# Kernel optimization log

Hardware: AMD Instinct MI355X
Metric: run time of the kernel (lower is better)

Reference implementation:

```python
import jax, jax.numpy as jnp
import numpy as np

N_NODES = 100000
N_GRAPHS = 512
HID = 128
IN_DIM = 128
OUT_DIM = 10
N_EDGES = 1600000


def gcn_conv(x, src, dst, W, b, n):
    # PyG GCNConv: add self-loops, symmetric normalization D^-1/2 (A+I) D^-1/2, then linear.
    h = x @ W  # [N, H]
    deg = jnp.zeros((n,), h.dtype).at[dst].add(1.0) + 1.0  # +1 self-loop
    dinv = jax.lax.rsqrt(deg)
    norm = dinv[src] * dinv[dst]  # [E]
    agg = jnp.zeros_like(h).at[dst].add(h[src] * norm[:, None])
    agg = agg + h * (dinv * dinv)[:, None]  # self-loop messages
    return agg + b


def setup_inputs() -> dict:
    key = jax.random.key(0)
    ks = jax.random.split(key, 12)
    x = jax.random.normal(ks[0], (N_NODES, IN_DIM), jnp.float32)
    edge_index = jax.random.randint(ks[1], (2, N_EDGES), 0, N_NODES)
    batch = jnp.sort(jax.random.randint(ks[2], (N_NODES,), 0, N_GRAPHS))
    def lin(k, fan_in, shape):
        bound = 1.0 / np.sqrt(fan_in)
        return jax.random.uniform(k, shape, jnp.float32, -bound, bound)
    W1 = lin(ks[3], IN_DIM, (IN_DIM, HID)); b1 = lin(ks[4], IN_DIM, (HID,))
    W2 = lin(ks[5], HID, (HID, HID)); b2 = lin(ks[6], HID, (HID,))
    W3 = lin(ks[7], HID, (HID, HID)); b3 = lin(ks[8], HID, (HID,))
    Wc1 = lin(ks[9], 2 * HID, (2 * HID, HID)); bc1 = lin(ks[9], 2 * HID, (HID,))
    Wc2 = lin(ks[10], HID, (HID, OUT_DIM)); bc2 = lin(ks[11], HID, (OUT_DIM,))
    return {"x": x, "edge_index": edge_index, "batch": batch,
            "W1": W1, "b1": b1, "W2": W2, "b2": b2, "W3": W3, "b3": b3,
            "Wc1": Wc1, "bc1": bc1, "Wc2": Wc2, "bc2": bc2}


def reference(x, edge_index, batch, W1, b1, W2, b2, W3, b3, Wc1, bc1, Wc2, bc2):
    src, dst = edge_index[0], edge_index[1]
    n = x.shape[0]
    h = jax.nn.relu(gcn_conv(x, src, dst, W1, b1, n))
    h = jax.nn.relu(gcn_conv(h, src, dst, W2, b2, n))
    h = gcn_conv(h, src, dst, W3, b3, n)  # no relu after last conv
    # global mean pool
    sums = jax.ops.segment_sum(h, batch, num_segments=N_GRAPHS)
    cnt = jax.ops.segment_sum(jnp.ones((n,), h.dtype), batch, num_segments=N_GRAPHS)
    mean = sums / jnp.maximum(cnt, 1.0)[:, None]
    # global max pool
    mx = jax.ops.segment_max(h, batch, num_segments=N_GRAPHS)
    mx = jnp.where(jnp.isfinite(mx), mx, 0.0)
    g = jnp.concatenate([mean, mx], axis=1)  # [G, 2H]
    g = jax.nn.relu(g @ Wc1 + bc1)
    return g @ Wc2 + bc2
```

## Files before the change

kernel.cpp:

```cpp
#include <hip/hip_runtime.h>

#define H 128
#define CAP 64
#define NB 256
#define BPCAP 6144
#define EPB 8192
#define SWLD 136

typedef __attribute__((ext_vector_type(8))) short bf16x8;
typedef __attribute__((ext_vector_type(4))) float f32x4;
typedef __attribute__((ext_vector_type(2))) float f32x2;

__device__ __forceinline__ unsigned short f2bf(float f) {
  unsigned u = __float_as_uint(f);
  unsigned r = u + 0x7FFFu + ((u >> 16) & 1u);
  return (unsigned short)(r >> 16);
}
__device__ __forceinline__ f32x2 up2(unsigned u) {
  return (f32x2){__uint_as_float(u << 16), __uint_as_float(u & 0xFFFF0000u)};
}

__global__ __launch_bounds__(256) void setup_all(
    const float* __restrict__ x,
    const float* __restrict__ W1, const float* __restrict__ W2, const float* __restrict__ W3,
    unsigned short* __restrict__ Xb, unsigned short* __restrict__ Wt,
    const int* __restrict__ batch, int* __restrict__ g_start, int G,
    unsigned short* __restrict__ P, unsigned short* __restrict__ Q,
    int* __restrict__ bcount,
    int n, int totalX4) {
  long long i = (long long)blockIdx.x * 256 + threadIdx.x;
  if (i < totalX4) {
    float4 v = *(const float4*)(x + i * 4);
    ushort4 o;
    o.x = f2bf(v.x); o.y = f2bf(v.y); o.z = f2bf(v.z); o.w = f2bf(v.w);
    *(ushort4*)(Xb + i * 4) = o;
    return;
  }
  i -= totalX4;
  if (i < 3 * H * H) {
    int w = (int)(i >> 14);
    int rem = (int)i & (H * H - 1);
    int c = rem >> 7;
    int k = rem & 127;
    const float* W = (w == 0) ? W1 : (w == 1) ? W2 : W3;
    Wt[i] = f2bf(W[(size_t)k * H + c]);
    return;
  }
  i -= 3 * H * H;
  if (i < n) {
    int ii = (int)i;
    int b = batch[ii];
    int prev = (ii == 0) ? -1 : batch[ii - 1];
    for (int g = prev + 1; g <= b; ++g) g_start[g] = ii;
    if (ii == n - 1) {
      for (int g = b + 1; g <= G; ++g) g_start[g] = n;
    }
    return;
  }
  i -= n;
  if (i < H) {
    P[(size_t)n * H + i] = 0;
    Q[(size_t)n * H + i] = 0;
    return;
  }
  i -= H;
  if (i < 512) bcount[i] = 0;
}

__global__ __launch_bounds__(512) void split1(
    const int* __restrict__ src, const int* __restrict__ dst,
    int2* __restrict__ buckets, int* __restrict__ bcount,
    int ne, int nbuck) {
  __shared__ int cnt[512];
  __shared__ int gbase[512];
  int tid = threadIdx.x;
  cnt[tid] = 0;
  __syncthreads();

  int beg = blockIdx.x * EPB;
  int end = beg + EPB; if (end > ne) end = ne;

  for (int e = beg + tid; e < end; e += 512) {
    int d = dst[e];
    atomicAdd(&cnt[d >> 8], 1);
  }
  __syncthreads();
  if (tid < nbuck) {
    int c = cnt[tid];
    gbase[tid] = (c > 0) ? atomicAdd(&bcount[tid], c) : 0;
    cnt[tid] = 0;
  }
  __syncthreads();
  for (int e = beg + tid; e < end; e += 512) {
    int s = src[e];
    int d = dst[e];
    int b = d >> 8;
    int l = atomicAdd(&cnt[b], 1);
    int pos = gbase[b] + l;
    if (pos < BPCAP) buckets[(size_t)b * BPCAP + pos] = make_int2(s, d);
  }
}

__global__ __launch_bounds__(512) void build_csr(
    const int2* __restrict__ buckets, const int* __restrict__ bcount,
    int* __restrict__ csr_src, int* __restrict__ deg, float* __restrict__ dinv,
    int n) {
  __shared__ int cur[NB];
  int b = blockIdx.x;
  int tid = threadIdx.x;
  if (tid < NB) cur[tid] = 0;
  __syncthreads();
  int cntb = bcount[b]; if (cntb > BPCAP) cntb = BPCAP;
  const int2* bp = buckets + (size_t)b * BPCAP;
  for (int i = tid; i < cntb; i += 512) {
    int2 e = bp[i];
    int slot = atomicAdd(&cur[e.y & (NB - 1)], 1);
    if (slot < CAP) csr_src[(size_t)e.y * CAP + slot] = e.x;
  }
  __syncthreads();
  if (tid < NB) {
    int node = b * NB + tid;
    if (node < n) {
      int d = cur[tid];
      deg[node] = d;
      dinv[node] = rsqrtf((float)(d + 1));
    }
  }
}

__global__ __launch_bounds__(256) void gemm_mfma(
    const unsigned short* __restrict__ Ab, const unsigned short* __restrict__ Wt,
    const float* __restrict__ dinv, unsigned short* __restrict__ outb, int n) {
  __shared__ unsigned short sW[H * SWLD];
  int tid = threadIdx.x;
  {
    int c = tid >> 1, hh = tid & 1;
    const int4* s = (const int4*)(Wt + (size_t)c * H + hh * 64);
    int4* d = (int4*)(sW + (size_t)c * SWLD + hh * 64);
#pragma unroll
    for (int i = 0; i < 8; ++i) d[i] = s[i];
  }
  __syncthreads();

  int wave = tid >> 6;
  int lane = tid & 63;
  int m = lane & 15;
  int quad = lane >> 4;
  int row = blockIdx.x * 64 + wave * 16 + m;
  bool rv = row < n;

  f32x4 acc[8];
#pragma unroll
  for (int t = 0; t < 8; ++t) acc[t] = (f32x4){0.f, 0.f, 0.f, 0.f};

  const unsigned short* arow = Ab + (size_t)(rv ? row : 0) * H;
#pragma unroll
  for (int k0 = 0; k0 < H; k0 += 32) {
    bf16x8 af;
    if (rv) af = *(const bf16x8*)(arow + k0 + quad * 8);
    else    af = (bf16x8){0, 0, 0, 0, 0, 0, 0, 0};
#pragma unroll
    for (int ct = 0; ct < 8; ++ct) {
      bf16x8 bfr = *(const bf16x8*)(sW + (size_t)(ct * 16 + m) * SWLD + k0 + quad * 8);
      acc[ct] = __builtin_amdgcn_mfma_f32_16x16x32_bf16(af, bfr, acc[ct], 0, 0, 0);
    }
  }

  __syncthreads();
  unsigned short (*sOut)[SWLD] = (unsigned short (*)[SWLD])sW;
  int r0 = wave * 16 + quad * 4;
#pragma unroll
  for (int r = 0; r < 4; ++r) {
    int orow = blockIdx.x * 64 + r0 + r;
    float dv = (orow < n) ? dinv[orow] : 0.f;
#pragma unroll
    for (int ct = 0; ct < 8; ++ct)
      sOut[r0 + r][ct * 16 + m] = f2bf(acc[ct][r] * dv);
  }
  __syncthreads();
  {
    int orow = blockIdx.x * 64 + (tid >> 2);
    if (orow < n) {
      const unsigned short* sp = &sOut[tid >> 2][(tid & 3) * 32];
      int4 t0 = *(const int4*)(sp + 0);
      int4 t1 = *(const int4*)(sp + 8);
      int4 t2 = *(const int4*)(sp + 16);
      int4 t3 = *(const int4*)(sp + 24);
      unsigned short* op = outb + (size_t)orow * H + (tid & 3) * 32;
      *(int4*)(op + 0)  = t0;
      *(int4*)(op + 8)  = t1;
      *(int4*)(op + 16) = t2;
      *(int4*)(op + 24) = t3;
    }
  }
}

template <bool RELU, bool OUTF32>
__global__ __launch_bounds__(256) void aggregate_bf(
    const unsigned short* __restrict__ hs, const int* __restrict__ deg_,
    const int* __restrict__ csr_src, const float* __restrict__ dinv,
    const float* __restrict__ b, void* __restrict__ outv, int n) {
  int node = blockIdx.x * 16 + (threadIdx.x >> 4);
  if (node >= n) return;
  int c = (threadIdx.x & 15) << 3;
  int deg = deg_[node]; if (deg > CAP) deg = CAP;
  int beg = node * CAP;
  int end = beg + ((deg + 7) & ~7);

  int4 sv = *(const int4*)(hs + (size_t)node * H + c);
  f32x2 a0 = up2(sv.x), a1 = up2(sv.y), a2 = up2(sv.z), a3 = up2(sv.w);

  int4 ia, ib;
  if (beg < end) {
    ia = *(const int4*)(csr_src + beg);
    ib = *(const int4*)(csr_src + beg + 4);
  }
  for (int k = beg; k < end; k += 8) {
    int4 ca = ia, cb = ib;
    int kn = k + 8;
    if (kn < end) {
      ia = *(const int4*)(csr_src + kn);
      ib = *(const int4*)(csr_src + kn + 4);
    }
    int rk = k - beg;
    if (rk + 8 > deg) {
      ca.x = (rk + 0 < deg) ? ca.x : n;
      ca.y = (rk + 1 < deg) ? ca.y : n;
      ca.z = (rk + 2 < deg) ? ca.z : n;
      ca.w = (rk + 3 < deg) ? ca.w : n;
      cb.x = (rk + 4 < deg) ? cb.x : n;
      cb.y = (rk + 5 < deg) ? cb.y : n;
      cb.z = (rk + 6 < deg) ? cb.z : n;
      cb.w = (rk + 7 < deg) ? cb.w : n;
    }
    int4 v0 = *(const int4*)(hs + (size_t)ca.x * H + c);
    int4 v1 = *(const int4*)(hs + (size_t)ca.y * H + c);
    int4 v2 = *(const int4*)(hs + (size_t)ca.z * H + c);
    int4 v3 = *(const int4*)(hs + (size_t)ca.w * H + c);
    int4 v4 = *(const int4*)(hs + (size_t)cb.x * H + c);
    int4 v5 = *(const int4*)(hs + (size_t)cb.y * H + c);
    int4 v6 = *(const int4*)(hs + (size_t)cb.z * H + c);
    int4 v7 = *(const int4*)(hs + (size_t)cb.w * H + c);
    a0 += ((up2(v0.x) + up2(v1.x)) + (up2(v2.x) + up2(v3.x))) +
          ((up2(v4.x) + up2(v5.x)) + (up2(v6.x) + up2(v7.x)));
    a1 += ((up2(v0.y) + up2(v1.y)) + (up2(v2.y) + up2(v3.y))) +
          ((up2(v4.y) + up2(v5.y)) + (up2(v6.y) + up2(v7.y)));
    a2 += ((up2(v0.z) + up2(v1.z)) + (up2(v2.z) + up2(v3.z))) +
          ((up2(v4.z) + up2(v5.z)) + (up2(v6.z) + up2(v7.z)));
    a3 += ((up2(v0.w) + up2(v1.w)) + (up2(v2.w) + up2(v3.w))) +
          ((up2(v4.w) + up2(v5.w)) + (up2(v6.w) + up2(v7.w)));
  }

  float dv = dinv[node];
  float4 b0 = *(const float4*)(b + c);
  float4 b1 = *(const float4*)(b + c + 4);
  float o0 = fmaf(a0.x, dv, b0.x), o1 = fmaf(a0.y, dv, b0.y);
  float o2 = fmaf(a1.x, dv, b0.z), o3 = fmaf(a1.y, dv, b0.w);
  float o4 = fmaf(a2.x, dv, b1.x), o5 = fmaf(a2.y, dv, b1.y);
  float o6 = fmaf(a3.x, dv, b1.z), o7 = fmaf(a3.y, dv, b1.w);
  if (RELU) {
    o0 = fmaxf(o0, 0.f); o1 = fmaxf(o1, 0.f); o2 = fmaxf(o2, 0.f); o3 = fmaxf(o3, 0.f);
    o4 = fmaxf(o4, 0.f); o5 = fmaxf(o5, 0.f); o6 = fmaxf(o6, 0.f); o7 = fmaxf(o7, 0.f);
  }
  if (OUTF32) {
    float* fo = (float*)outv + (size_t)node * H + c;
    *(float4*)(fo + 0) = make_float4(o0, o1, o2, o3);
    *(float4*)(fo + 4) = make_float4(o4, o5, o6, o7);
  } else {
    int4 ob;
    ob.x = ((unsigned)f2bf(o1) << 16) | f2bf(o0);
    ob.y = ((unsigned)f2bf(o3) << 16) | f2bf(o2);
    ob.z = ((unsigned)f2bf(o5) << 16) | f2bf(o4);
    ob.w = ((unsigned)f2bf(o7) << 16) | f2bf(o6);
    *(int4*)((unsigned short*)outv + (size_t)node * H + c) = ob;
  }
}

__global__ __launch_bounds__(256) void pool2(
    const float* __restrict__ h, const int* __restrict__ g_start,
    float* __restrict__ gmean, float* __restrict__ gmax, int n) {
  __shared__ float ssum[16][64];
  __shared__ float smax[16][64];
  int g = blockIdx.x >> 1;
  int half = blockIdx.x & 1;
  int beg = g_start[g];
  int end = g_start[g + 1];
  int q = threadIdx.x >> 4;
  int c = (threadIdx.x & 15) << 2;
  int cg = half * 64 + c;

  float4 s = make_float4(0.f, 0.f, 0.f, 0.f);
  float4 m = make_float4(-INFINITY, -INFINITY, -INFINITY, -INFINITY);
  for (int node = beg + q; node < end; node += 16) {
    float4 v = *(const float4*)(h + (size_t)node * H + cg);
    s.x += v.x; s.y += v.y; s.z += v.z; s.w += v.w;
    m.x = fmaxf(m.x, v.x); m.y = fmaxf(m.y, v.y);
    m.z = fmaxf(m.z, v.z); m.w = fmaxf(m.w, v.w);
  }
  *(float4*)&ssum[q][c] = s;
  *(float4*)&smax[q][c] = m;
  __syncthreads();

  int cnt = end - beg;
  int t = threadIdx.x;
  if (t < 64) {
    float tot = 0.f;
#pragma unroll
    for (int qq = 0; qq < 16; ++qq) tot += ssum[qq][t];
    gmean[(size_t)g * H + half * 64 + t] = tot / fmaxf((float)cnt, 1.0f);
  } else if (t < 128) {
    int cc = t - 64;
    float mx = -INFINITY;
#pragma unroll
    for (int qq = 0; qq < 16; ++qq) mx = fmaxf(mx, smax[qq][cc]);
    gmax[(size_t)g * H + half * 64 + cc] = (cnt == 0) ? 0.0f : mx;
  }
}

__global__ __launch_bounds__(128) void classify_kernel(
    const float* __restrict__ gmean, const float* __restrict__ gmax,
    const float* __restrict__ Wc1, const float* __restrict__ bc1,
    const float* __restrict__ Wc2, const float* __restrict__ bc2,
    float* __restrict__ out) {
  __shared__ float gv[2 * H];
  __shared__ float hid[H];
  int gid = blockIdx.x;
  int t = threadIdx.x;
  gv[t] = gmean[(size_t)gid * H + t];
  gv[H + t] = gmax[(size_t)gid * H + t];
  __syncthreads();
  float acc = 0.f;
#pragma unroll 8
  for (int k = 0; k < 2 * H; ++k) acc = fmaf(gv[k], Wc1[(size_t)k * H + t], acc);
  hid[t] = fmaxf(acc + bc1[t], 0.f);
  __syncthreads();
  if (t < 10) {
    float a2 = 0.f;
    for (int j = 0; j < H; ++j) a2 = fmaf(hid[j], Wc2[(size_t)j * 10 + t], a2);
    out[(size_t)gid * 10 + t] = a2 + bc2[t];
  }
}

extern "C" void kernel_launch(void* const* d_in, const int* in_sizes, int n_in,
                              void* d_out, int out_size, void* d_ws, size_t ws_size,
                              hipStream_t stream) {
  const float* x    = (const float*)d_in[0];
  const int* ei     = (const int*)d_in[1];
  const int* batch  = (const int*)d_in[2];
  const float* W1   = (const float*)d_in[3];
  const float* b1   = (const float*)d_in[4];
  const float* W2   = (const float*)d_in[5];
  const float* b2   = (const float*)d_in[6];
  const float* W3   = (const float*)d_in[7];
  const float* b3   = (const float*)d_in[8];
  const float* Wc1  = (const float*)d_in[9];
  const float* bc1  = (const float*)d_in[10];
  const float* Wc2  = (const float*)d_in[11];
  const float* bc2  = (const float*)d_in[12];
  float* out = (float*)d_out;

  const int n  = in_sizes[2];
  const int ne = in_sizes[1] / 2;
  const int G  = 512;
  const size_t NFb = (size_t)(n + 1) * H;

  const int* src = ei;
  const int* dst = ei + ne;

  unsigned short* P_bf = (unsigned short*)d_ws;
  unsigned short* Q_bf = P_bf + NFb;
  float*          F2f  = (float*)(Q_bf + NFb);
  unsigned short* Xb   = (unsigned short*)F2f;
  int* csr_src = (int*)(F2f + (size_t)n * H);
  const size_t csr_cap = (size_t)n * CAP;
  char* p = (char*)(csr_src + csr_cap);
  int*            deg      = (int*)p;            p += (size_t)n * 4;
  float*          dinv     = (float*)p;          p += (size_t)n * 4;
  int*            g_start  = (int*)p;            p += (size_t)(G + 1) * 4;
  float*          gmean    = (float*)p;          p += (size_t)G * H * 4;
  float*          gmax     = (float*)p;          p += (size_t)G * H * 4;
  p = (char*)(((uintptr_t)p + 255) & ~(uintptr_t)255);
  unsigned short* Wt       = (unsigned short*)p; p += (size_t)3 * H * H * 2;
  int*            bcount   = (int*)p;            p += 512 * 4;
  int2*           buckets  = (int2*)Q_bf;

  const int nbuck = (n + NB - 1) / NB;

  {
    int totalX4 = n * H / 4;
    long long tot = (long long)totalX4 + 3 * H * H + n + H + 512;
    int blocks = (int)((tot + 255) / 256);
    setup_all<<<blocks, 256, 0, stream>>>(x, W1, W2, W3, Xb, Wt,
                                          batch, g_start, G,
                                          P_bf, Q_bf, bcount, n, totalX4);
  }

  split1<<<(ne + EPB - 1) / EPB, 512, 0, stream>>>(src, dst, buckets, bcount, ne, nbuck);
  build_csr<<<nbuck, 512, 0, stream>>>(buckets, bcount, csr_src, deg, dinv, n);

  const int tile_grid = (n + 63) / 64;
  const int node_grid = (n + 15) / 16;

  gemm_mfma<<<tile_grid, 256, 0, stream>>>(Xb, Wt, dinv, Q_bf, n);
  aggregate_bf<true, false><<<node_grid, 256, 0, stream>>>(Q_bf, deg, csr_src, dinv, b1, P_bf, n);

  gemm_mfma<<<tile_grid, 256, 0, stream>>>(P_bf, Wt + H * H, dinv, Q_bf, n);
  aggregate_bf<true, false><<<node_grid, 256, 0, stream>>>(Q_bf, deg, csr_src, dinv, b2, P_bf, n);

  gemm_mfma<<<tile_grid, 256, 0, stream>>>(P_bf, Wt + 2 * H * H, dinv, Q_bf, n);
  aggregate_bf<false, true><<<node_grid, 256, 0, stream>>>(Q_bf, deg, csr_src, dinv, b3, F2f, n);

  pool2<<<2 * G, 256, 0, stream>>>(F2f, g_start, gmean, gmax, n);
  classify_kernel<<<G, 128, 0, stream>>>(gmean, gmax, Wc1, bc1, Wc2, bc2, out);
}
```

Baseline: 431.8 us.

## Fuse fp32-to-bf16 input cast into first GEMM and stage CSR rows in LDS

Drops the separate pass that converts x to bf16 and instead converts fp32 loads to bf16 inside the first GEMM, avoiding a full write and re-read of the input features. The bucket sort uses smaller buckets (128 nodes), and its global bucket counters are padded 16 ints apart to reduce atomic contention. build_csr now assembles each bucket's adjacency rows in shared memory and writes them out with coalesced int4 stores instead of scattered stores. In exchange, each bucket's capacity is much smaller, so overflow is more likely with skewed degree distributions, and build_csr now uses 32KB of LDS per block.

```diff
diff --git a/kernel.cpp b/kernel.cpp
--- a/kernel.cpp
+++ b/kernel.cpp
@@ -2,9 +2,9 @@
 
 #define H 128
 #define CAP 64
-#define NB 256
-#define BPCAP 6144
-#define EPB 8192
+#define NB 128
+#define BPCAP 2560
+#define EPB 4096
 #define SWLD 136
 
 typedef __attribute__((ext_vector_type(8))) short bf16x8;
@@ -21,22 +21,12 @@
 }
 
 __global__ __launch_bounds__(256) void setup_all(
-    const float* __restrict__ x,
     const float* __restrict__ W1, const float* __restrict__ W2, const float* __restrict__ W3,
-    unsigned short* __restrict__ Xb, unsigned short* __restrict__ Wt,
+    unsigned short* __restrict__ Wt,
     const int* __restrict__ batch, int* __restrict__ g_start, int G,
     unsigned short* __restrict__ P, unsigned short* __restrict__ Q,
-    int* __restrict__ bcount,
-    int n, int totalX4) {
+    int* __restrict__ bcount, int nbc, int n) {
   long long i = (long long)blockIdx.x * 256 + threadIdx.x;
-  if (i < totalX4) {
-    float4 v = *(const float4*)(x + i * 4);
-    ushort4 o;
-    o.x = f2bf(v.x); o.y = f2bf(v.y); o.z = f2bf(v.z); o.w = f2bf(v.w);
-    *(ushort4*)(Xb + i * 4) = o;
-    return;
-  }
-  i -= totalX4;
   if (i < 3 * H * H) {
     int w = (int)(i >> 14);
     int rem = (int)i & (H * H - 1);
@@ -64,17 +54,17 @@
     return;
   }
   i -= H;
-  if (i < 512) bcount[i] = 0;
+  if (i < nbc) bcount[i] = 0;
 }
 
 __global__ __launch_bounds__(512) void split1(
     const int* __restrict__ src, const int* __restrict__ dst,
     int2* __restrict__ buckets, int* __restrict__ bcount,
     int ne, int nbuck) {
-  __shared__ int cnt[512];
-  __shared__ int gbase[512];
+  __shared__ int cnt[1024];
+  __shared__ int gbase[1024];
   int tid = threadIdx.x;
-  cnt[tid] = 0;
+  cnt[tid] = 0; cnt[tid + 512] = 0;
   __syncthreads();
 
   int beg = blockIdx.x * EPB;
@@ -82,19 +72,19 @@
 
   for (int e = beg + tid; e < end; e += 512) {
     int d = dst[e];
-    atomicAdd(&cnt[d >> 8], 1);
-  }
-  __syncthreads();
-  if (tid < nbuck) {
-    int c = cnt[tid];
-    gbase[tid] = (c > 0) ? atomicAdd(&bcount[tid], c) : 0;
-    cnt[tid] = 0;
+    atomicAdd(&cnt[d >> 7], 1);
+  }
+  __syncthreads();
+  for (int i = tid; i < nbuck; i += 512) {
+    int c = cnt[i];
+    gbase[i] = (c > 0) ? atomicAdd(&bcount[i * 16], c) : 0;
+    cnt[i] = 0;
   }
   __syncthreads();
   for (int e = beg + tid; e < end; e += 512) {
     int s = src[e];
     int d = dst[e];
-    int b = d >> 8;
+    int b = d >> 7;
     int l = atomicAdd(&cnt[b], 1);
     int pos = gbase[b] + l;
     if (pos < BPCAP) buckets[(size_t)b * BPCAP + pos] = make_int2(s, d);
@@ -105,19 +95,25 @@
     const int2* __restrict__ buckets, const int* __restrict__ bcount,
     int* __restrict__ csr_src, int* __restrict__ deg, float* __restrict__ dinv,
     int n) {
+  __shared__ int rows[NB * CAP];
   __shared__ int cur[NB];
   int b = blockIdx.x;
   int tid = threadIdx.x;
   if (tid < NB) cur[tid] = 0;
   __syncthreads();
-  int cntb = bcount[b]; if (cntb > BPCAP) cntb = BPCAP;
+  int cntb = bcount[b * 16]; if (cntb > BPCAP) cntb = BPCAP;
   const int2* bp = buckets + (size_t)b * BPCAP;
   for (int i = tid; i < cntb; i += 512) {
     int2 e = bp[i];
-    int slot = atomicAdd(&cur[e.y & (NB - 1)], 1);
-    if (slot < CAP) csr_src[(size_t)e.y * CAP + slot] = e.x;
-  }
-  __syncthreads();
+    int r = e.y & (NB - 1);
+    int slot = atomicAdd(&cur[r], 1);
+    if (slot < CAP) rows[r * CAP + slot] = e.x;
+  }
+  __syncthreads();
+  int4* gdst = (int4*)(csr_src + (size_t)b * NB * CAP);
+  const int4* lsrc = (const int4*)rows;
+#pragma unroll
+  for (int i = tid; i < NB * CAP / 4; i += 512) gdst[i] = lsrc[i];
   if (tid < NB) {
     int node = b * NB + tid;
     if (node < n) {
@@ -128,8 +124,9 @@
   }
 }
 
+template <bool AF32>
 __global__ __launch_bounds__(256) void gemm_mfma(
-    const unsigned short* __restrict__ Ab, const unsigned short* __restrict__ Wt,
+    const void* __restrict__ Av, const unsigned short* __restrict__ Wt,
     const float* __restrict__ dinv, unsigned short* __restrict__ outb, int n) {
   __shared__ unsigned short sW[H * SWLD];
   int tid = threadIdx.x;
@@ -153,12 +150,25 @@
 #pragma unroll
   for (int t = 0; t < 8; ++t) acc[t] = (f32x4){0.f, 0.f, 0.f, 0.f};
 
-  const unsigned short* arow = Ab + (size_t)(rv ? row : 0) * H;
 #pragma unroll
   for (int k0 = 0; k0 < H; k0 += 32) {
     bf16x8 af;
-    if (rv) af = *(const bf16x8*)(arow + k0 + quad * 8);
-    else    af = (bf16x8){0, 0, 0, 0, 0, 0, 0, 0};
+    if (rv) {
+      if (AF32) {
+        const float* arow = (const float*)Av + (size_t)row * H + k0 + quad * 8;
+        float4 f0 = *(const float4*)(arow + 0);
+        float4 f1 = *(const float4*)(arow + 4);
+        af[0] = (short)f2bf(f0.x); af[1] = (short)f2bf(f0.y);
+        af[2] = (short)f2bf(f0.z); af[3] = (short)f2bf(f0.w);
+        af[4] = (short)f2bf(f1.x); af[5] = (short)f2bf(f1.y);
+        af[6] = (short)f2bf(f1.z); af[7] = (short)f2bf(f1.w);
+      } else {
+        const unsigned short* arow = (const unsigned short*)Av + (size_t)row * H;
+        af = *(const bf16x8*)(arow + k0 + quad * 8);
+      }
+    } else {
+      af = (bf16x8){0, 0, 0, 0, 0, 0, 0, 0};
+    }
 #pragma unroll
     for (int ct = 0; ct < 8; ++ct) {
       bf16x8 bfr = *(const bf16x8*)(sW + (size_t)(ct * 16 + m) * SWLD + k0 + quad * 8);
@@ -367,12 +377,14 @@
   const int* src = ei;
   const int* dst = ei + ne;
 
+  const int nbuck = (n + NB - 1) / NB;
+  const int nbc   = nbuck * 16;
+
   unsigned short* P_bf = (unsigned short*)d_ws;
   unsigned short* Q_bf = P_bf + NFb;
   float*          F2f  = (float*)(Q_bf + NFb);
-  unsigned short* Xb   = (unsigned short*)F2f;
   int* csr_src = (int*)(F2f + (size_t)n * H);
-  const size_t csr_cap = (size_t)n * CAP;
+  const size_t csr_cap = (size_t)nbuck * NB * CAP;
   char* p = (char*)(csr_src + csr_cap);
   int*            deg      = (int*)p;            p += (size_t)n * 4;
   float*          dinv     = (float*)p;          p += (size_t)n * 4;
@@ -381,18 +393,15 @@
   float*          gmax     = (float*)p;          p += (size_t)G * H * 4;
   p = (char*)(((uintptr_t)p + 255) & ~(uintptr_t)255);
   unsigned short* Wt       = (unsigned short*)p; p += (size_t)3 * H * H * 2;
-  int*            bcount   = (int*)p;            p += 512 * 4;
+  p = (char*)(((uintptr_t)p + 63) & ~(uintptr_t)63);
+  int*            bcount   = (int*)p;            p += (size_t)nbc * 4;
   int2*           buckets  = (int2*)Q_bf;
 
-  const int nbuck = (n + NB - 1) / NB;
-
   {
-    int totalX4 = n * H / 4;
-    long long tot = (long long)totalX4 + 3 * H * H + n + H + 512;
+    long long tot = (long long)3 * H * H + n + H + nbc;
     int blocks = (int)((tot + 255) / 256);
-    setup_all<<<blocks, 256, 0, stream>>>(x, W1, W2, W3, Xb, Wt,
-                                          batch, g_start, G,
-                                          P_bf, Q_bf, bcount, n, totalX4);
+    setup_all<<<blocks, 256, 0, stream>>>(W1, W2, W3, Wt, batch, g_start, G,
+                                          P_bf, Q_bf, bcount, nbc, n);
   }
 
   split1<<<(ne + EPB - 1) / EPB, 512, 0, stream>>>(src, dst, buckets, bcount, ne, nbuck);
@@ -401,13 +410,13 @@
   const int tile_grid = (n + 63) / 64;
   const int node_grid = (n + 15) / 16;
 
-  gemm_mfma<<<tile_grid, 256, 0, stream>>>(Xb, Wt, dinv, Q_bf, n);
+  gemm_mfma<true><<<tile_grid, 256, 0, stream>>>(x, Wt, dinv, Q_bf, n);
   aggregate_bf<true, false><<<node_grid, 256, 0, stream>>>(Q_bf, deg, csr_src, dinv, b1, P_bf, n);
 
-  gemm_mfma<<<tile_grid, 256, 0, stream>>>(P_bf, Wt + H * H, dinv, Q_bf, n);
+  gemm_mfma<false><<<tile_grid, 256, 0, stream>>>(P_bf, Wt + H * H, dinv, Q_bf, n);
   aggregate_bf<true, false><<<node_grid, 256, 0, stream>>>(Q_bf, deg, csr_src, dinv, b2, P_bf, n);
 
-  gemm_mfma<<<tile_grid, 256, 0, stream>>>(P_bf, Wt + 2 * H * H, dinv, Q_bf, n);
+  gemm_mfma<false><<<tile_grid, 256, 0, stream>>>(P_bf, Wt + 2 * H * H, dinv, Q_bf, n);
   aggregate_bf<false, true><<<node_grid, 256, 0, stream>>>(Q_bf, deg, csr_src, dinv, b3, F2f, n);
 
   pool2<<<2 * G, 256, 0, stream>>>(F2f, g_start, gmean, gmax, n);
```

Measured after the change: 440.9 us. 1.02x slower.

## Slice node features into 16-column planes and fuse input bf16 cast into GEMM

Applied to the files above, without the earlier changes.

Stores hidden features as 8 column slices of 16 bf16 values per node, each plane 32 bytes per row. Aggregation blocks now each handle one slice over 128 nodes, so a slice's gathers come from a smaller 3.2 MB plane that fits better in cache. The first GEMM now reads fp32 x directly and converts it to bf16 in registers, which removes the separate conversion pass and its buffer. The cost is 32-byte gathers instead of full 256-byte rows, and the CSR index list is re-read eight times, once per slice.

```diff
diff --git a/kernel.cpp b/kernel.cpp
--- a/kernel.cpp
+++ b/kernel.cpp
@@ -11,6 +11,7 @@
 typedef __attribute__((ext_vector_type(4))) float f32x4;
 typedef __attribute__((ext_vector_type(2))) float f32x2;
 
+
 __device__ __forceinline__ unsigned short f2bf(float f) {
   unsigned u = __float_as_uint(f);
   unsigned r = u + 0x7FFFu + ((u >> 16) & 1u);
@@ -21,22 +22,12 @@
 }
 
 __global__ __launch_bounds__(256) void setup_all(
-    const float* __restrict__ x,
     const float* __restrict__ W1, const float* __restrict__ W2, const float* __restrict__ W3,
-    unsigned short* __restrict__ Xb, unsigned short* __restrict__ Wt,
+    unsigned short* __restrict__ Wt,
     const int* __restrict__ batch, int* __restrict__ g_start, int G,
     unsigned short* __restrict__ P, unsigned short* __restrict__ Q,
-    int* __restrict__ bcount,
-    int n, int totalX4) {
+    int* __restrict__ bcount, int n) {
   long long i = (long long)blockIdx.x * 256 + threadIdx.x;
-  if (i < totalX4) {
-    float4 v = *(const float4*)(x + i * 4);
-    ushort4 o;
-    o.x = f2bf(v.x); o.y = f2bf(v.y); o.z = f2bf(v.z); o.w = f2bf(v.w);
-    *(ushort4*)(Xb + i * 4) = o;
-    return;
-  }
-  i -= totalX4;
   if (i < 3 * H * H) {
     int w = (int)(i >> 14);
     int rem = (int)i & (H * H - 1);
@@ -59,8 +50,10 @@
   }
   i -= n;
   if (i < H) {
-    P[(size_t)n * H + i] = 0;
-    Q[(size_t)n * H + i] = 0;
+    size_t SS = (size_t)(n + 1) * 16;
+    int s = (int)(i >> 4), o = (int)(i & 15);
+    P[(size_t)s * SS + (size_t)n * 16 + o] = 0;
+    Q[(size_t)s * SS + (size_t)n * 16 + o] = 0;
     return;
   }
   i -= H;
@@ -128,10 +121,12 @@
   }
 }
 
+template <bool AF32>
 __global__ __launch_bounds__(256) void gemm_mfma(
-    const unsigned short* __restrict__ Ab, const unsigned short* __restrict__ Wt,
+    const void* __restrict__ Av, const unsigned short* __restrict__ Wt,
     const float* __restrict__ dinv, unsigned short* __restrict__ outb, int n) {
   __shared__ unsigned short sW[H * SWLD];
+  size_t SS = (size_t)(n + 1) * 16;
   int tid = threadIdx.x;
   {
     int c = tid >> 1, hh = tid & 1;
@@ -153,12 +148,27 @@
 #pragma unroll
   for (int t = 0; t < 8; ++t) acc[t] = (f32x4){0.f, 0.f, 0.f, 0.f};
 
-  const unsigned short* arow = Ab + (size_t)(rv ? row : 0) * H;
 #pragma unroll
   for (int k0 = 0; k0 < H; k0 += 32) {
     bf16x8 af;
-    if (rv) af = *(const bf16x8*)(arow + k0 + quad * 8);
-    else    af = (bf16x8){0, 0, 0, 0, 0, 0, 0, 0};
+    if (rv) {
+      if (AF32) {
+        const float* arow = (const float*)Av + (size_t)row * H + k0 + quad * 8;
+        float4 f0 = *(const float4*)(arow + 0);
+        float4 f1 = *(const float4*)(arow + 4);
+        af[0] = (short)f2bf(f0.x); af[1] = (short)f2bf(f0.y);
+        af[2] = (short)f2bf(f0.z); af[3] = (short)f2bf(f0.w);
+        af[4] = (short)f2bf(f1.x); af[5] = (short)f2bf(f1.y);
+        af[6] = (short)f2bf(f1.z); af[7] = (short)f2bf(f1.w);
+      } else {
+        int gcol = k0 + quad * 8;
+        const unsigned short* arow = (const unsigned short*)Av +
+            (size_t)(gcol >> 4) * SS + (size_t)row * 16 + (gcol & 15);
+        af = *(const bf16x8*)(arow);
+      }
+    } else {
+      af = (bf16x8){0, 0, 0, 0, 0, 0, 0, 0};
+    }
 #pragma unroll
     for (int ct = 0; ct < 8; ++ct) {
       bf16x8 bfr = *(const bf16x8*)(sW + (size_t)(ct * 16 + m) * SWLD + k0 + quad * 8);
@@ -182,32 +192,34 @@
     int orow = blockIdx.x * 64 + (tid >> 2);
     if (orow < n) {
       const unsigned short* sp = &sOut[tid >> 2][(tid & 3) * 32];
-      int4 t0 = *(const int4*)(sp + 0);
-      int4 t1 = *(const int4*)(sp + 8);
-      int4 t2 = *(const int4*)(sp + 16);
-      int4 t3 = *(const int4*)(sp + 24);
-      unsigned short* op = outb + (size_t)orow * H + (tid & 3) * 32;
-      *(int4*)(op + 0)  = t0;
-      *(int4*)(op + 8)  = t1;
-      *(int4*)(op + 16) = t2;
-      *(int4*)(op + 24) = t3;
+      int s0 = (tid & 3) * 2;
+      unsigned short* o0 = outb + (size_t)s0 * SS + (size_t)orow * 16;
+      unsigned short* o1 = o0 + SS;
+      *(int4*)(o0 + 0) = *(const int4*)(sp + 0);
+      *(int4*)(o0 + 8) = *(const int4*)(sp + 8);
+      *(int4*)(o1 + 0) = *(const int4*)(sp + 16);
+      *(int4*)(o1 + 8) = *(const int4*)(sp + 24);
     }
   }
 }
 
 template <bool RELU, bool OUTF32>
-__global__ __launch_bounds__(256) void aggregate_bf(
+__global__ __launch_bounds__(256) void aggregate_sl(
     const unsigned short* __restrict__ hs, const int* __restrict__ deg_,
     const int* __restrict__ csr_src, const float* __restrict__ dinv,
     const float* __restrict__ b, void* __restrict__ outv, int n) {
-  int node = blockIdx.x * 16 + (threadIdx.x >> 4);
+  int slice = blockIdx.x & 7;
+  int blk = blockIdx.x >> 3;
+  int node = blk * 128 + (threadIdx.x >> 1);
   if (node >= n) return;
-  int c = (threadIdx.x & 15) << 3;
+  size_t SS = (size_t)(n + 1) * 16;
+  const unsigned short* T = hs + (size_t)slice * SS;
+  int c8 = (threadIdx.x & 1) << 3;
   int deg = deg_[node]; if (deg > CAP) deg = CAP;
   int beg = node * CAP;
   int end = beg + ((deg + 7) & ~7);
 
-  int4 sv = *(const int4*)(hs + (size_t)node * H + c);
+  int4 sv = *(const int4*)(T + (size_t)node * 16 + c8);
   f32x2 a0 = up2(sv.x), a1 = up2(sv.y), a2 = up2(sv.z), a3 = up2(sv.w);
 
   int4 ia, ib;
@@ -233,14 +245,14 @@
       cb.z = (rk + 6 < deg) ? cb.z : n;
       cb.w = (rk + 7 < deg) ? cb.w : n;
     }
-    int4 v0 = *(const int4*)(hs + (size_t)ca.x * H + c);
-    int4 v1 = *(const int4*)(hs + (size_t)ca.y * H + c);
-    int4 v2 = *(const int4*)(hs + (size_t)ca.z * H + c);
-    int4 v3 = *(const int4*)(hs + (size_t)ca.w * H + c);
-    int4 v4 = *(const int4*)(hs + (size_t)cb.x * H + c);
-    int4 v5 = *(const int4*)(hs + (size_t)cb.y * H + c);
-    int4 v6 = *(const int4*)(hs + (size_t)cb.z * H + c);
-    int4 v7 = *(const int4*)(hs + (size_t)cb.w * H + c);
+    int4 v0 = *(const int4*)(T + (size_t)ca.x * 16 + c8);
+    int4 v1 = *(const int4*)(T + (size_t)ca.y * 16 + c8);
+    int4 v2 = *(const int4*)(T + (size_t)ca.z * 16 + c8);
+    int4 v3 = *(const int4*)(T + (size_t)ca.w * 16 + c8);
+    int4 v4 = *(const int4*)(T + (size_t)cb.x * 16 + c8);
+    int4 v5 = *(const int4*)(T + (size_t)cb.y * 16 + c8);
+    int4 v6 = *(const int4*)(T + (size_t)cb.z * 16 + c8);
+    int4 v7 = *(const int4*)(T + (size_t)cb.w * 16 + c8);
     a0 += ((up2(v0.x) + up2(v1.x)) + (up2(v2.x) + up2(v3.x))) +
           ((up2(v4.x) + up2(v5.x)) + (up2(v6.x) + up2(v7.x)));
     a1 += ((up2(v0.y) + up2(v1.y)) + (up2(v2.y) + up2(v3.y))) +
@@ -252,8 +264,9 @@
   }
 
   float dv = dinv[node];
-  float4 b0 = *(const float4*)(b + c);
-  float4 b1 = *(const float4*)(b + c + 4);
+  int gc = slice * 16 + c8;
+  float4 b0 = *(const float4*)(b + gc);
+  float4 b1 = *(const float4*)(b + gc + 4);
   float o0 = fmaf(a0.x, dv, b0.x), o1 = fmaf(a0.y, dv, b0.y);
   float o2 = fmaf(a1.x, dv, b0.z), o3 = fmaf(a1.y, dv, b0.w);
   float o4 = fmaf(a2.x, dv, b1.x), o5 = fmaf(a2.y, dv, b1.y);
@@ -263,7 +276,7 @@
     o4 = fmaxf(o4, 0.f); o5 = fmaxf(o5, 0.f); o6 = fmaxf(o6, 0.f); o7 = fmaxf(o7, 0.f);
   }
   if (OUTF32) {
-    float* fo = (float*)outv + (size_t)node * H + c;
+    float* fo = (float*)outv + (size_t)slice * n * 16 + (size_t)node * 16 + c8;
     *(float4*)(fo + 0) = make_float4(o0, o1, o2, o3);
     *(float4*)(fo + 4) = make_float4(o4, o5, o6, o7);
   } else {
@@ -272,7 +285,7 @@
     ob.y = ((unsigned)f2bf(o3) << 16) | f2bf(o2);
     ob.z = ((unsigned)f2bf(o5) << 16) | f2bf(o4);
     ob.w = ((unsigned)f2bf(o7) << 16) | f2bf(o6);
-    *(int4*)((unsigned short*)outv + (size_t)node * H + c) = ob;
+    *(int4*)((unsigned short*)outv + (size_t)slice * SS + (size_t)node * 16 + c8) = ob;
   }
 }
 
@@ -288,11 +301,12 @@
   int q = threadIdx.x >> 4;
   int c = (threadIdx.x & 15) << 2;
   int cg = half * 64 + c;
+  const float* base = h + (size_t)(cg >> 4) * n * 16 + (cg & 15);
 
   float4 s = make_float4(0.f, 0.f, 0.f, 0.f);
   float4 m = make_float4(-INFINITY, -INFINITY, -INFINITY, -INFINITY);
   for (int node = beg + q; node < end; node += 16) {
-    float4 v = *(const float4*)(h + (size_t)node * H + cg);
+    float4 v = *(const float4*)(base + (size_t)node * 16);
     s.x += v.x; s.y += v.y; s.z += v.z; s.w += v.w;
     m.x = fmaxf(m.x, v.x); m.y = fmaxf(m.y, v.y);
     m.z = fmaxf(m.z, v.z); m.w = fmaxf(m.w, v.w);
@@ -370,7 +384,6 @@
   unsigned short* P_bf = (unsigned short*)d_ws;
   unsigned short* Q_bf = P_bf + NFb;
   float*          F2f  = (float*)(Q_bf + NFb);
-  unsigned short* Xb   = (unsigned short*)F2f;
   int* csr_src = (int*)(F2f + (size_t)n * H);
   const size_t csr_cap = (size_t)n * CAP;
   char* p = (char*)(csr_src + csr_cap);
@@ -382,33 +395,31 @@
   p = (char*)(((uintptr_t)p + 255) & ~(uintptr_t)255);
   unsigned short* Wt       = (unsigned short*)p; p += (size_t)3 * H * H * 2;
   int*            bcount   = (int*)p;            p += 512 * 4;
-  int2*           buckets  = (int2*)Q_bf;
+  int2*           buckets  = (int2*)F2f;
 
   const int nbuck = (n + NB - 1) / NB;
 
   {
-    int totalX4 = n * H / 4;
-    long long tot = (long long)totalX4 + 3 * H * H + n + H + 512;
+    long long tot = (long long)3 * H * H + n + H + 512;
     int blocks = (int)((tot + 255) / 256);
-    setup_all<<<blocks, 256, 0, stream>>>(x, W1, W2, W3, Xb, Wt,
-                                          batch, g_start, G,
-                                          P_bf, Q_bf, bcount, n, totalX4);
+    setup_all<<<blocks, 256, 0, stream>>>(W1, W2, W3, Wt, batch, g_start, G,
+                                          P_bf, Q_bf, bcount, n);
   }
 
   split1<<<(ne + EPB - 1) / EPB, 512, 0, stream>>>(src, dst, buckets, bcount, ne, nbuck);
   build_csr<<<nbuck, 512, 0, stream>>>(buckets, bcount, csr_src, deg, dinv, n);
 
   const int tile_grid = (n + 63) / 64;
-  const int node_grid = (n + 15) / 16;
-
-  gemm_mfma<<<tile_grid, 256, 0, stream>>>(Xb, Wt, dinv, Q_bf, n);
-  aggregate_bf<true, false><<<node_grid, 256, 0, stream>>>(Q_bf, deg, csr_src, dinv, b1, P_bf, n);
-
-  gemm_mfma<<<tile_grid, 256, 0, stream>>>(P_bf, Wt + H * H, dinv, Q_bf, n);
-  aggregate_bf<true, false><<<node_grid, 256, 0, stream>>>(Q_bf, deg, csr_src, dinv, b2, P_bf, n);
-
-  gemm_mfma<<<tile_grid, 256, 0, stream>>>(P_bf, Wt + 2 * H * H, dinv, Q_bf, n);
-  aggregate_bf<false, true><<<node_grid, 256, 0, stream>>>(Q_bf, deg, csr_src, dinv, b3, F2f, n);
+  const int agg_grid  = ((n + 127) / 128) * 8;
+
+  gemm_mfma<true><<<tile_grid, 256, 0, stream>>>(x, Wt, dinv, Q_bf, n);
+  aggregate_sl<true, false><<<agg_grid, 256, 0, stream>>>(Q_bf, deg, csr_src, dinv, b1, P_bf, n);
+
+  gemm_mfma<false><<<tile_grid, 256, 0, stream>>>(P_bf, Wt + H * H, dinv, Q_bf, n);
+  aggregate_sl<true, false><<<agg_grid, 256, 0, stream>>>(Q_bf, deg, csr_src, dinv, b2, P_bf, n);
+
+  gemm_mfma<false><<<tile_grid, 256, 0, stream>>>(P_bf, Wt + 2 * H * H, dinv, Q_bf, n);
+  aggregate_sl<false, true><<<agg_grid, 256, 0, stream>>>(Q_bf, deg, csr_src, dinv, b3, F2f, n);
 
   pool2<<<2 * G, 256, 0, stream>>>(F2f, g_start, gmean, gmax, n);
   classify_kernel<<<G, 128, 0, stream>>>(gmean, gmax, Wc1, bc1, Wc2, bc2, out);
```

Result: slower. 493.6 us (+14.3%).

## Fuse last aggregation into pooling and degree-sort nodes within buckets

Applied to the files above, without the earlier changes.

The third-layer aggregation is merged into the pooling kernel, so the final fp32 node features are never written to memory and read back. Each pool block now does the neighbour gather for the nodes of its graph directly. Separately, build_csr now produces a permutation that sorts nodes by degree inside each 256-node bucket, and the aggregate kernel visits nodes in that order so the 16 nodes sharing a block have similar loop lengths. The fused kernel uses only 1024 blocks, each walking a whole graph, which may lower occupancy and load balance compared with the per-node grid. The permutation also loses some locality on output writes.

```diff
diff --git a/kernel.cpp b/kernel.cpp
--- a/kernel.cpp
+++ b/kernel.cpp
@@ -104,11 +104,14 @@
 __global__ __launch_bounds__(512) void build_csr(
     const int2* __restrict__ buckets, const int* __restrict__ bcount,
     int* __restrict__ csr_src, int* __restrict__ deg, float* __restrict__ dinv,
-    int n) {
+    int* __restrict__ perm, int n) {
   __shared__ int cur[NB];
+  __shared__ int bcnt[CAP + 1];
+  __shared__ int bbase[CAP + 1];
   int b = blockIdx.x;
   int tid = threadIdx.x;
   if (tid < NB) cur[tid] = 0;
+  if (tid >= NB && tid < NB + CAP + 1) bcnt[tid - NB] = 0;
   __syncthreads();
   int cntb = bcount[b]; if (cntb > BPCAP) cntb = BPCAP;
   const int2* bp = buckets + (size_t)b * BPCAP;
@@ -118,13 +121,26 @@
     if (slot < CAP) csr_src[(size_t)e.y * CAP + slot] = e.x;
   }
   __syncthreads();
-  if (tid < NB) {
-    int node = b * NB + tid;
-    if (node < n) {
-      int d = cur[tid];
-      deg[node] = d;
-      dinv[node] = rsqrtf((float)(d + 1));
-    }
+  int node = b * NB + tid;
+  bool valid = (tid < NB) && (node < n);
+  int d = 0;
+  if (valid) {
+    int dr = cur[tid];
+    deg[node] = dr;
+    dinv[node] = rsqrtf((float)(dr + 1));
+    d = (dr > CAP) ? CAP : dr;
+    atomicAdd(&bcnt[d], 1);
+  }
+  if (tid < NB) perm[b * NB + tid] = n;
+  __syncthreads();
+  if (tid == 0) {
+    int acc = 0;
+    for (int i = 0; i <= CAP; ++i) { bbase[i] = acc; acc += bcnt[i]; }
+  }
+  __syncthreads();
+  if (valid) {
+    int r = atomicAdd(&bbase[d], 1);
+    perm[b * NB + r] = node;
   }
 }
 
@@ -195,12 +211,14 @@
   }
 }
 
-template <bool RELU, bool OUTF32>
 __global__ __launch_bounds__(256) void aggregate_bf(
     const unsigned short* __restrict__ hs, const int* __restrict__ deg_,
     const int* __restrict__ csr_src, const float* __restrict__ dinv,
-    const float* __restrict__ b, void* __restrict__ outv, int n) {
-  int node = blockIdx.x * 16 + (threadIdx.x >> 4);
+    const float* __restrict__ b, unsigned short* __restrict__ outv,
+    const int* __restrict__ perm, int n, int npad) {
+  int idx = blockIdx.x * 16 + (threadIdx.x >> 4);
+  if (idx >= npad) return;
+  int node = perm[idx];
   if (node >= n) return;
   int c = (threadIdx.x & 15) << 3;
   int deg = deg_[node]; if (deg > CAP) deg = CAP;
@@ -254,51 +272,99 @@
   float dv = dinv[node];
   float4 b0 = *(const float4*)(b + c);
   float4 b1 = *(const float4*)(b + c + 4);
-  float o0 = fmaf(a0.x, dv, b0.x), o1 = fmaf(a0.y, dv, b0.y);
-  float o2 = fmaf(a1.x, dv, b0.z), o3 = fmaf(a1.y, dv, b0.w);
-  float o4 = fmaf(a2.x, dv, b1.x), o5 = fmaf(a2.y, dv, b1.y);
-  float o6 = fmaf(a3.x, dv, b1.z), o7 = fmaf(a3.y, dv, b1.w);
-  if (RELU) {
-    o0 = fmaxf(o0, 0.f); o1 = fmaxf(o1, 0.f); o2 = fmaxf(o2, 0.f); o3 = fmaxf(o3, 0.f);
-    o4 = fmaxf(o4, 0.f); o5 = fmaxf(o5, 0.f); o6 = fmaxf(o6, 0.f); o7 = fmaxf(o7, 0.f);
-  }
-  if (OUTF32) {
-    float* fo = (float*)outv + (size_t)node * H + c;
-    *(float4*)(fo + 0) = make_float4(o0, o1, o2, o3);
-    *(float4*)(fo + 4) = make_float4(o4, o5, o6, o7);
-  } else {
-    int4 ob;
-    ob.x = ((unsigned)f2bf(o1) << 16) | f2bf(o0);
-    ob.y = ((unsigned)f2bf(o3) << 16) | f2bf(o2);
-    ob.z = ((unsigned)f2bf(o5) << 16) | f2bf(o4);
-    ob.w = ((unsigned)f2bf(o7) << 16) | f2bf(o6);
-    *(int4*)((unsigned short*)outv + (size_t)node * H + c) = ob;
-  }
-}
-
-__global__ __launch_bounds__(256) void pool2(
-    const float* __restrict__ h, const int* __restrict__ g_start,
+  float o0 = fmaxf(fmaf(a0.x, dv, b0.x), 0.f), o1 = fmaxf(fmaf(a0.y, dv, b0.y), 0.f);
+  float o2 = fmaxf(fmaf(a1.x, dv, b0.z), 0.f), o3 = fmaxf(fmaf(a1.y, dv, b0.w), 0.f);
+  float o4 = fmaxf(fmaf(a2.x, dv, b1.x), 0.f), o5 = fmaxf(fmaf(a2.y, dv, b1.y), 0.f);
+  float o6 = fmaxf(fmaf(a3.x, dv, b1.z), 0.f), o7 = fmaxf(fmaf(a3.y, dv, b1.w), 0.f);
+  int4 ob;
+  ob.x = ((unsigned)f2bf(o1) << 16) | f2bf(o0);
+  ob.y = ((unsigned)f2bf(o3) << 16) | f2bf(o2);
+  ob.z = ((unsigned)f2bf(o5) << 16) | f2bf(o4);
+  ob.w = ((unsigned)f2bf(o7) << 16) | f2bf(o6);
+  *(int4*)(outv + (size_t)node * H + c) = ob;
+}
+
+__global__ __launch_bounds__(256) void agg_pool(
+    const unsigned short* __restrict__ hs, const int* __restrict__ deg_,
+    const int* __restrict__ csr_src, const float* __restrict__ dinv,
+    const float* __restrict__ b, const int* __restrict__ g_start,
     float* __restrict__ gmean, float* __restrict__ gmax, int n) {
-  __shared__ float ssum[16][64];
-  __shared__ float smax[16][64];
+  __shared__ float ssum[32][64];
+  __shared__ float smax[32][64];
   int g = blockIdx.x >> 1;
   int half = blockIdx.x & 1;
   int beg = g_start[g];
   int end = g_start[g + 1];
-  int q = threadIdx.x >> 4;
-  int c = (threadIdx.x & 15) << 2;
-  int cg = half * 64 + c;
-
-  float4 s = make_float4(0.f, 0.f, 0.f, 0.f);
-  float4 m = make_float4(-INFINITY, -INFINITY, -INFINITY, -INFINITY);
-  for (int node = beg + q; node < end; node += 16) {
-    float4 v = *(const float4*)(h + (size_t)node * H + cg);
-    s.x += v.x; s.y += v.y; s.z += v.z; s.w += v.w;
-    m.x = fmaxf(m.x, v.x); m.y = fmaxf(m.y, v.y);
-    m.z = fmaxf(m.z, v.z); m.w = fmaxf(m.w, v.w);
-  }
-  *(float4*)&ssum[q][c] = s;
-  *(float4*)&smax[q][c] = m;
+  int grp = threadIdx.x >> 3;
+  int lc = (threadIdx.x & 7) << 3;
+  int cg = half * 64 + lc;
+
+  float4 bb0 = *(const float4*)(b + cg);
+  float4 bb1 = *(const float4*)(b + cg + 4);
+  float s0 = 0, s1 = 0, s2 = 0, s3 = 0, s4 = 0, s5 = 0, s6 = 0, s7 = 0;
+  float m0 = -INFINITY, m1 = -INFINITY, m2 = -INFINITY, m3 = -INFINITY;
+  float m4 = -INFINITY, m5 = -INFINITY, m6 = -INFINITY, m7 = -INFINITY;
+
+  for (int node = beg + grp; node < end; node += 32) {
+    int deg = deg_[node]; if (deg > CAP) deg = CAP;
+    int kb = node * CAP;
+    int ke = kb + ((deg + 7) & ~7);
+    int4 sv = *(const int4*)(hs + (size_t)node * H + cg);
+    f32x2 a0 = up2(sv.x), a1 = up2(sv.y), a2 = up2(sv.z), a3 = up2(sv.w);
+    int4 ia, ib;
+    if (kb < ke) {
+      ia = *(const int4*)(csr_src + kb);
+      ib = *(const int4*)(csr_src + kb + 4);
+    }
+    for (int k = kb; k < ke; k += 8) {
+      int4 ca = ia, cb = ib;
+      int kn = k + 8;
+      if (kn < ke) {
+        ia = *(const int4*)(csr_src + kn);
+        ib = *(const int4*)(csr_src + kn + 4);
+      }
+      int rk = k - kb;
+      if (rk + 8 > deg) {
+        ca.x = (rk + 0 < deg) ? ca.x : n;
+        ca.y = (rk + 1 < deg) ? ca.y : n;
+        ca.z = (rk + 2 < deg) ? ca.z : n;
+        ca.w = (rk + 3 < deg) ? ca.w : n;
+        cb.x = (rk + 4 < deg) ? cb.x : n;
+        cb.y = (rk + 5 < deg) ? cb.y : n;
+        cb.z = (rk + 6 < deg) ? cb.z : n;
+        cb.w = (rk + 7 < deg) ? cb.w : n;
+      }
+      int4 v0 = *(const int4*)(hs + (size_t)ca.x * H + cg);
+      int4 v1 = *(const int4*)(hs + (size_t)ca.y * H + cg);
+      int4 v2 = *(const int4*)(hs + (size_t)ca.z * H + cg);
+      int4 v3 = *(const int4*)(hs + (size_t)ca.w * H + cg);
+      int4 v4 = *(const int4*)(hs + (size_t)cb.x * H + cg);
+      int4 v5 = *(const int4*)(hs + (size_t)cb.y * H + cg);
+      int4 v6 = *(const int4*)(hs + (size_t)cb.z * H + cg);
+      int4 v7 = *(const int4*)(hs + (size_t)cb.w * H + cg);
+      a0 += ((up2(v0.x) + up2(v1.x)) + (up2(v2.x) + up2(v3.x))) +
+            ((up2(v4.x) + up2(v5.x)) + (up2(v6.x) + up2(v7.x)));
+      a1 += ((up2(v0.y) + up2(v1.y)) + (up2(v2.y) + up2(v3.y))) +
+            ((up2(v4.y) + up2(v5.y)) + (up2(v6.y) + up2(v7.y)));
+      a2 += ((up2(v0.z) + up2(v1.z)) + (up2(v2.z) + up2(v3.z))) +
+            ((up2(v4.z) + up2(v5.z)) + (up2(v6.z) + up2(v7.z)));
+      a3 += ((up2(v0.w) + up2(v1.w)) + (up2(v2.w) + up2(v3.w))) +
+            ((up2(v4.w) + up2(v5.w)) + (up2(v6.w) + up2(v7.w)));
+    }
+    float dv = dinv[node];
+    float o0 = fmaf(a0.x, dv, bb0.x), o1 = fmaf(a0.y, dv, bb0.y);
+    float o2 = fmaf(a1.x, dv, bb0.z), o3 = fmaf(a1.y, dv, bb0.w);
+    float o4 = fmaf(a2.x, dv, bb1.x), o5 = fmaf(a2.y, dv, bb1.y);
+    float o6 = fmaf(a3.x, dv, bb1.z), o7 = fmaf(a3.y, dv, bb1.w);
+    s0 += o0; s1 += o1; s2 += o2; s3 += o3; s4 += o4; s5 += o5; s6 += o6; s7 += o7;
+    m0 = fmaxf(m0, o0); m1 = fmaxf(m1, o1); m2 = fmaxf(m2, o2); m3 = fmaxf(m3, o3);
+    m4 = fmaxf(m4, o4); m5 = fmaxf(m5, o5); m6 = fmaxf(m6, o6); m7 = fmaxf(m7, o7);
+  }
+
+  *(float4*)&ssum[grp][lc]     = make_float4(s0, s1, s2, s3);
+  *(float4*)&ssum[grp][lc + 4] = make_float4(s4, s5, s6, s7);
+  *(float4*)&smax[grp][lc]     = make_float4(m0, m1, m2, m3);
+  *(float4*)&smax[grp][lc + 4] = make_float4(m4, m5, m6, m7);
   __syncthreads();
 
   int cnt = end - beg;
@@ -306,13 +372,13 @@
   if (t < 64) {
     float tot = 0.f;
 #pragma unroll
-    for (int qq = 0; qq < 16; ++qq) tot += ssum[qq][t];
+    for (int qq = 0; qq < 32; ++qq) tot += ssum[qq][t];
     gmean[(size_t)g * H + half * 64 + t] = tot / fmaxf((float)cnt, 1.0f);
   } else if (t < 128) {
     int cc = t - 64;
     float mx = -INFINITY;
 #pragma unroll
-    for (int qq = 0; qq < 16; ++qq) mx = fmaxf(mx, smax[qq][cc]);
+    for (int qq = 0; qq < 32; ++qq) mx = fmaxf(mx, smax[qq][cc]);
     gmax[(size_t)g * H + half * 64 + cc] = (cnt == 0) ? 0.0f : mx;
   }
 }
@@ -367,11 +433,13 @@
   const int* src = ei;
   const int* dst = ei + ne;
 
+  const int nbuck = (n + NB - 1) / NB;
+  const int npad  = nbuck * NB;
+
   unsigned short* P_bf = (unsigned short*)d_ws;
   unsigned short* Q_bf = P_bf + NFb;
-  float*          F2f  = (float*)(Q_bf + NFb);
-  unsigned short* Xb   = (unsigned short*)F2f;
-  int* csr_src = (int*)(F2f + (size_t)n * H);
+  unsigned short* Xb   = Q_bf + NFb;
+  int* csr_src = (int*)(Xb + (size_t)n * H);
   const size_t csr_cap = (size_t)n * CAP;
   char* p = (char*)(csr_src + csr_cap);
   int*            deg      = (int*)p;            p += (size_t)n * 4;
@@ -379,12 +447,11 @@
   int*            g_start  = (int*)p;            p += (size_t)(G + 1) * 4;
   float*          gmean    = (float*)p;          p += (size_t)G * H * 4;
   float*          gmax     = (float*)p;          p += (size_t)G * H * 4;
+  int*            perm     = (int*)p;            p += (size_t)npad * 4;
   p = (char*)(((uintptr_t)p + 255) & ~(uintptr_t)255);
   unsigned short* Wt       = (unsigned short*)p; p += (size_t)3 * H * H * 2;
   int*            bcount   = (int*)p;            p += 512 * 4;
   int2*           buckets  = (int2*)Q_bf;
-
-  const int nbuck = (n + NB - 1) / NB;
 
   {
     int totalX4 = n * H / 4;
@@ -396,20 +463,19 @@
   }
 
   split1<<<(ne + EPB - 1) / EPB, 512, 0, stream>>>(src, dst, buckets, bcount, ne, nbuck);
-  build_csr<<<nbuck, 512, 0, stream>>>(buckets, bcount, csr_src, deg, dinv, n);
+  build_csr<<<nbuck, 512, 0, stream>>>(buckets, bcount, csr_src, deg, dinv, perm, n);
 
   const int tile_grid = (n + 63) / 64;
-  const int node_grid = (n + 15) / 16;
+  const int node_grid = npad / 16;
 
   gemm_mfma<<<tile_grid, 256, 0, stream>>>(Xb, Wt, dinv, Q_bf, n);
-  aggregate_bf<true, false><<<node_grid, 256, 0, stream>>>(Q_bf, deg, csr_src, dinv, b1, P_bf, n);
+  aggregate_bf<<<node_grid, 256, 0, stream>>>(Q_bf, deg, csr_src, dinv, b1, P_bf, perm, n, npad);
 
   gemm_mfma<<<tile_grid, 256, 0, stream>>>(P_bf, Wt + H * H, dinv, Q_bf, n);
-  aggregate_bf<true, false><<<node_grid, 256, 0, stream>>>(Q_bf, deg, csr_src, dinv, b2, P_bf, n);
+  aggregate_bf<<<node_grid, 256, 0, stream>>>(Q_bf, deg, csr_src, dinv, b2, P_bf, perm, n, npad);
 
   gemm_mfma<<<tile_grid, 256, 0, stream>>>(P_bf, Wt + 2 * H * H, dinv, Q_bf, n);
-  aggregate_bf<false, true><<<node_grid, 256, 0, stream>>>(Q_bf, deg, csr_src, dinv, b3, F2f, n);
-
-  pool2<<<2 * G, 256, 0, stream>>>(F2f, g_start, gmean, gmax, n);
+  agg_pool<<<2 * G, 256, 0, stream>>>(Q_bf, deg, csr_src, dinv, b3, g_start, gmean, gmax, n);
+
   classify_kernel<<<G, 128, 0, stream>>>(gmean, gmax, Wc1, bc1, Wc2, bc2, out);
 }
```

Result: no change. 429.2 us (-0.6%).
